# Performance work log

Measured on AMD Instinct MI355X. Metric: run time of the kernel, lower is better.

## Reference

```python
import jax, jax.numpy as jnp
import numpy as np

B, S, F, H = 64, 100, 128, 8
D = F // H
SCALE = D ** -0.5


def setup_inputs() -> dict:
    key = jax.random.key(0)
    ks = jax.random.split(key, 12)
    def lin(k, fan_in, fan_out):
        bound = 1.0 / np.sqrt(fan_in)
        kw, kb = jax.random.split(k)
        W = jax.random.uniform(kw, (fan_in, fan_out), minval=-bound, maxval=bound, dtype=jnp.float32)
        b = jax.random.uniform(kb, (fan_out,), minval=-bound, maxval=bound, dtype=jnp.float32)
        return W, b
    Wq, bq = lin(ks[0], F, F)
    Wk, bk = lin(ks[1], F, F)
    Wv, bv = lin(ks[2], F, F)
    Wo, bo = lin(ks[3], F, F)
    q = jax.random.normal(ks[4], (B, S, F), dtype=jnp.float32)
    k = jax.random.normal(ks[5], (B, S, F), dtype=jnp.float32)
    v = jax.random.normal(ks[6], (B, S, F), dtype=jnp.float32)
    # causal mask broadcast over heads: 1 = keep, 0 = masked
    mask = jnp.tril(jnp.ones((S, S), dtype=jnp.float32))[None, None, :, :].repeat(B, axis=0)
    return {"q": q, "k": k, "v": v, "mask": mask,
            "Wq": Wq, "bq": bq, "Wk": Wk, "bk": bk,
            "Wv": Wv, "bv": bv, "Wo": Wo, "bo": bo}


def reference(q, k, v, mask, Wq, bq, Wk, bk, Wv, bv, Wo, bo):
    # project and split heads: [B,S,F] -> [B,H,S,D]
    def heads(x, W, b):
        y = x @ W + b
        return y.reshape(B, S, H, D).transpose(0, 2, 1, 3)
    qh = heads(q, Wq, bq)
    kh = heads(k, Wk, bk)
    vh = heads(v, Wv, bv)
    scores = jnp.einsum('bhqd,bhkd->bhqk', qh, kh) * SCALE
    scores = jnp.where(mask == 0, -1e9, scores)
    attn = jax.nn.softmax(scores, axis=-1)
    out = jnp.einsum('bhqk,bhkd->bhqd', attn, vh)
    out = out.transpose(0, 2, 1, 3).reshape(B, S, F)
    return out @ Wo + bo
```

## Files before the change

### kernel.cpp

```cpp
#include <hip/hip_runtime.h>
#include <hip/hip_bf16.h>

typedef __attribute__((ext_vector_type(8))) short bf16x8;
typedef __attribute__((ext_vector_type(4))) float f32x4;
typedef __attribute__((ext_vector_type(4))) unsigned short us4;

#define Bb 64
#define Ss 100
#define Ff 128
#define Hh 8
#define Dd 16
#define ROWS (Bb * Ss)
#define ELEMS (ROWS * Ff)

__device__ __forceinline__ unsigned short f2bf(float f) {
    unsigned u = __float_as_uint(f);
    u += 0x7FFFu + ((u >> 16) & 1u);
    return (unsigned short)(u >> 16);
}

__global__ __launch_bounds__(256) void convert_w_kernel(
    const float* __restrict__ Wq, const float* __restrict__ Wk,
    const float* __restrict__ Wv, const float* __restrict__ Wo,
    unsigned short* __restrict__ Wt)
{
    const int wsel = blockIdx.x >> 3, kb = blockIdx.x & 7;
    const float* W = wsel == 0 ? Wq : wsel == 1 ? Wk : wsel == 2 ? Wv : Wo;
    unsigned short* T = Wt + wsel * 16384;
    const int t = threadIdx.x;
    const int n  = t >> 1;
    const int k0 = kb * 16 + (t & 1) * 8;
    bf16x8 v;
#pragma unroll
    for (int j = 0; j < 8; ++j) v[j] = (short)f2bf(W[(k0 + j) * Ff + n]);
    *(bf16x8*)&T[n * Ff + k0] = v;
}

__device__ __forceinline__ void mfma_gemm(const unsigned short* Xs,
                                          const unsigned short* Ws,
                                          f32x4 acc[8], int w, int m, int g)
{
#pragma unroll
    for (int kk = 0; kk < 128; kk += 32) {
        bf16x8 a = *(const bf16x8*)&Xs[(w * 16 + m) * 136 + kk + g * 8];
#pragma unroll
        for (int n = 0; n < 8; ++n) {
            bf16x8 b = *(const bf16x8*)&Ws[(n * 16 + m) * 136 + kk + g * 8];
            acc[n] = __builtin_amdgcn_mfma_f32_16x16x32_bf16(a, b, acc[n], 0, 0, 0);
        }
    }
}

__global__ __launch_bounds__(256) void proj_qkv_kernel(
    const float* __restrict__ q, const float* __restrict__ k, const float* __restrict__ v,
    const unsigned short* __restrict__ Wt,
    const float* __restrict__ bq, const float* __restrict__ bk, const float* __restrict__ bv,
    unsigned short* __restrict__ Qh, unsigned short* __restrict__ Kh, unsigned short* __restrict__ Vh)
{
    __shared__ unsigned short Xs[64 * 136];
    __shared__ unsigned short Ws[128 * 136];
    const int p = blockIdx.y;
    const float* X               = p == 0 ? q  : p == 1 ? k  : v;
    const unsigned short* Wg     = Wt + p * 16384;
    const float* bias            = p == 0 ? bq : p == 1 ? bk : bv;
    unsigned short* OUT          = p == 0 ? Qh : p == 1 ? Kh : Vh;
    const int t = threadIdx.x;
    const int r0 = blockIdx.x * 64;

#pragma unroll
    for (int i = 0; i < 8; ++i) {
        int idx = t + i * 256;
        int r = idx >> 5, c4 = (idx & 31) * 4;
        float4 xv = *(const float4*)&X[(r0 + r) * Ff + c4];
        us4 s4;
        s4[0] = f2bf(xv.x); s4[1] = f2bf(xv.y);
        s4[2] = f2bf(xv.z); s4[3] = f2bf(xv.w);
        *(us4*)&Xs[r * 136 + c4] = s4;
    }
#pragma unroll
    for (int i = 0; i < 8; ++i) {
        int r = (t >> 4) + i * 16, c8 = (t & 15) * 8;
        *(bf16x8*)&Ws[r * 136 + c8] = *(const bf16x8*)&Wg[r * Ff + c8];
    }
    __syncthreads();

    const int w = t >> 6, lane = t & 63, m = lane & 15, g = lane >> 4;
    f32x4 zz = {0.f, 0.f, 0.f, 0.f};
    f32x4 acc[8];
#pragma unroll
    for (int n = 0; n < 8; ++n) acc[n] = zz;
    mfma_gemm(Xs, Ws, acc, w, m, g);

#pragma unroll
    for (int n = 0; n < 8; ++n) {
        float bb = bias[n * 16 + m];
#pragma unroll
        for (int r = 0; r < 4; ++r) {
            int row = r0 + w * 16 + g * 4 + r;
            unsigned b = (unsigned)row / 100u;
            unsigned s = (unsigned)row - b * 100u;
            OUT[((b * 8u + n) * 100u + s) * 16u + m] = f2bf(acc[n][r] + bb);
        }
    }
}

__global__ __launch_bounds__(448) void attn_kernel(
    const unsigned short* __restrict__ Qh, const unsigned short* __restrict__ Kh,
    const unsigned short* __restrict__ Vh, unsigned short* __restrict__ ao)
{
    __shared__ unsigned short lds[24576];
    unsigned short* Qs = lds;
    unsigned short* Ks = lds + 3584;
    unsigned short* Vt = lds + 7168;
    unsigned short* Ps = lds + 9344;

    const int bh = blockIdx.x, b = bh >> 3, h = bh & 7;
    const int t = threadIdx.x;

    for (int i = t; i < 3072; i += 448) ((int4*)lds)[i] = make_int4(0, 0, 0, 0);
    __syncthreads();

    const unsigned short* Qg = Qh + bh * 1600;
    const unsigned short* Kg = Kh + bh * 1600;
    const unsigned short* Vg = Vh + bh * 1600;
    for (int i = t; i < 400; i += 448) {
        int s = i >> 2, d0 = (i & 3) * 4;
        *(us4*)&Qs[s * 32 + d0] = *(const us4*)&Qg[i * 4];
        *(us4*)&Ks[s * 32 + d0] = *(const us4*)&Kg[i * 4];
        us4 vv = *(const us4*)&Vg[i * 4];
        Vt[(d0 + 0) * 136 + s] = vv[0];
        Vt[(d0 + 1) * 136 + s] = vv[1];
        Vt[(d0 + 2) * 136 + s] = vv[2];
        Vt[(d0 + 3) * 136 + s] = vv[3];
    }
    __syncthreads();

    const int w = t >> 6, lane = t & 63, m = lane & 15, g = lane >> 4;
    f32x4 zz = {0.f, 0.f, 0.f, 0.f};

    bf16x8 aq = *(const bf16x8*)&Qs[(w * 16 + m) * 32 + g * 8];
    f32x4 sc[7];
#pragma unroll
    for (int tt = 0; tt < 7; ++tt) {
        bf16x8 bk = *(const bf16x8*)&Ks[(tt * 16 + m) * 32 + g * 8];
        sc[tt] = __builtin_amdgcn_mfma_f32_16x16x32_bf16(aq, bk, zz, 0, 0, 0);
    }

    const int rbase = w * 16 + g * 4;
    float mx[4], sum[4], invl[4];
#pragma unroll
    for (int r = 0; r < 4; ++r) mx[r] = -3.0e38f;
#pragma unroll
    for (int tt = 0; tt < 7; ++tt)
#pragma unroll
        for (int r = 0; r < 4; ++r) {
            float sv = (tt * 16 + m <= rbase + r) ? sc[tt][r] * 0.25f : -1.0e30f;
            sc[tt][r] = sv;
            mx[r] = fmaxf(mx[r], sv);
        }
#pragma unroll
    for (int off = 1; off < 16; off <<= 1)
#pragma unroll
        for (int r = 0; r < 4; ++r) mx[r] = fmaxf(mx[r], __shfl_xor(mx[r], off));
#pragma unroll
    for (int r = 0; r < 4; ++r) sum[r] = 0.f;

    unsigned short* Pw = Ps + w * 2176;
#pragma unroll
    for (int tt = 0; tt < 7; ++tt)
#pragma unroll
        for (int r = 0; r < 4; ++r) {
            float e = __expf(sc[tt][r] - mx[r]);
            sum[r] += e;
            Pw[(g * 4 + r) * 136 + tt * 16 + m] = f2bf(e);
        }
#pragma unroll
    for (int off = 1; off < 16; off <<= 1)
#pragma unroll
        for (int r = 0; r < 4; ++r) sum[r] += __shfl_xor(sum[r], off);
#pragma unroll
    for (int r = 0; r < 4; ++r) invl[r] = 1.0f / sum[r];

    f32x4 oacc = zz;
#pragma unroll
    for (int kk = 0; kk < 128; kk += 32) {
        bf16x8 ap = *(const bf16x8*)&Pw[m * 136 + kk + g * 8];
        bf16x8 bv = *(const bf16x8*)&Vt[m * 136 + kk + g * 8];
        oacc = __builtin_amdgcn_mfma_f32_16x16x32_bf16(ap, bv, oacc, 0, 0, 0);
    }
#pragma unroll
    for (int r = 0; r < 4; ++r) {
        int s = rbase + r;
        if (s < Ss)
            ao[(b * Ss + s) * Ff + h * 16 + m] = f2bf(oacc[r] * invl[r]);
    }
}

__global__ __launch_bounds__(256) void proj_out_kernel(
    const unsigned short* __restrict__ ao, const unsigned short* __restrict__ WtO,
    const float* __restrict__ bo, float* __restrict__ out)
{
    __shared__ unsigned short Xs[64 * 136];
    __shared__ unsigned short Ws[128 * 136];
    const int t = threadIdx.x;
    const int r0 = blockIdx.x * 64;
#pragma unroll
    for (int i = 0; i < 4; ++i) {
        int idx = t + i * 256;
        int r = idx >> 4, c8 = (idx & 15) * 8;
        *(bf16x8*)&Xs[r * 136 + c8] = *(const bf16x8*)&ao[(r0 + r) * Ff + c8];
    }
#pragma unroll
    for (int i = 0; i < 8; ++i) {
        int r = (t >> 4) + i * 16, c8 = (t & 15) * 8;
        *(bf16x8*)&Ws[r * 136 + c8] = *(const bf16x8*)&WtO[r * Ff + c8];
    }
    __syncthreads();

    const int w = t >> 6, lane = t & 63, m = lane & 15, g = lane >> 4;
    f32x4 zz = {0.f, 0.f, 0.f, 0.f};
    f32x4 acc[8];
#pragma unroll
    for (int n = 0; n < 8; ++n) acc[n] = zz;
    mfma_gemm(Xs, Ws, acc, w, m, g);

#pragma unroll
    for (int n = 0; n < 8; ++n) {
        float bb = bo[n * 16 + m];
#pragma unroll
        for (int r = 0; r < 4; ++r) {
            int row = r0 + w * 16 + g * 4 + r;
            out[row * Ff + n * 16 + m] = acc[n][r] + bb;
        }
    }
}

extern "C" void kernel_launch(void* const* d_in, const int* in_sizes, int n_in,
                              void* d_out, int out_size, void* d_ws, size_t ws_size,
                              hipStream_t stream) {
    const float* q  = (const float*)d_in[0];
    const float* k  = (const float*)d_in[1];
    const float* v  = (const float*)d_in[2];
    const float* Wq = (const float*)d_in[4];
    const float* bq = (const float*)d_in[5];
    const float* Wk = (const float*)d_in[6];
    const float* bk = (const float*)d_in[7];
    const float* Wv = (const float*)d_in[8];
    const float* bv = (const float*)d_in[9];
    const float* Wo = (const float*)d_in[10];
    const float* bo = (const float*)d_in[11];

    float* out = (float*)d_out;
    unsigned short* wsu = (unsigned short*)d_ws;
    unsigned short* Wt = wsu;
    unsigned short* Qh = wsu + 65536;
    unsigned short* Kh = Qh + ELEMS;
    unsigned short* Vh = Kh + ELEMS;
    unsigned short* ao = Vh + ELEMS;

    convert_w_kernel<<<dim3(32), dim3(256), 0, stream>>>(Wq, Wk, Wv, Wo, Wt);
    proj_qkv_kernel<<<dim3(100, 3), dim3(256), 0, stream>>>(
        q, k, v, Wt, bq, bk, bv, Qh, Kh, Vh);
    attn_kernel<<<dim3(512), dim3(448), 0, stream>>>(Qh, Kh, Vh, ao);
    proj_out_kernel<<<dim3(100), dim3(256), 0, stream>>>(ao, Wt + 3 * 16384, bo, out);
}
```

Before: 98.29 us.

## Fuse QKV projection into per-head attention kernel and fold weight conversion

Merges the QKV projection into the attention kernel. Each (batch, head) block now loads its 16-column slices of Wq/Wk/Wv, projects q/k/v rows straight from fp32 global memory with MFMA, and keeps Q, K and transposed V in LDS. The Wo transpose and conversion moves into 8 extra blocks of the same launch. This removes two launches and the Qh/Kh/Vh round trip through global memory. In exchange, each head block re-reads the full q/k/v rows, so global input traffic rises about 8x across heads, and it does strided scalar weight loads and a larger LDS footprint.

```diff
diff --git a/kernel.cpp b/kernel.cpp
--- a/kernel.cpp
+++ b/kernel.cpp
@@ -3,13 +3,11 @@
 
 typedef __attribute__((ext_vector_type(8))) short bf16x8;
 typedef __attribute__((ext_vector_type(4))) float f32x4;
-typedef __attribute__((ext_vector_type(4))) unsigned short us4;
 
 #define Bb 64
 #define Ss 100
 #define Ff 128
 #define Hh 8
-#define Dd 16
 #define ROWS (Bb * Ss)
 #define ELEMS (ROWS * Ff)
 
@@ -19,131 +17,97 @@
     return (unsigned short)(u >> 16);
 }
 
-__global__ __launch_bounds__(256) void convert_w_kernel(
-    const float* __restrict__ Wq, const float* __restrict__ Wk,
-    const float* __restrict__ Wv, const float* __restrict__ Wo,
-    unsigned short* __restrict__ Wt)
+__device__ __forceinline__ bf16x8 load_a8(const float* p) {
+    float4 x0 = *(const float4*)p;
+    float4 x1 = *(const float4*)(p + 4);
+    bf16x8 a;
+    a[0] = (short)f2bf(x0.x); a[1] = (short)f2bf(x0.y);
+    a[2] = (short)f2bf(x0.z); a[3] = (short)f2bf(x0.w);
+    a[4] = (short)f2bf(x1.x); a[5] = (short)f2bf(x1.y);
+    a[6] = (short)f2bf(x1.z); a[7] = (short)f2bf(x1.w);
+    return a;
+}
+
+__global__ __launch_bounds__(448) void fused_qkv_attn_kernel(
+    const float* __restrict__ q, const float* __restrict__ k, const float* __restrict__ v,
+    const float* __restrict__ Wq, const float* __restrict__ bq,
+    const float* __restrict__ Wk, const float* __restrict__ bk,
+    const float* __restrict__ Wv, const float* __restrict__ bv,
+    const float* __restrict__ Wo,
+    unsigned short* __restrict__ ao, unsigned short* __restrict__ WtO)
 {
-    const int wsel = blockIdx.x >> 3, kb = blockIdx.x & 7;
-    const float* W = wsel == 0 ? Wq : wsel == 1 ? Wk : wsel == 2 ? Wv : Wo;
-    unsigned short* T = Wt + wsel * 16384;
+    const int blk = blockIdx.x;
     const int t = threadIdx.x;
-    const int n  = t >> 1;
-    const int k0 = kb * 16 + (t & 1) * 8;
-    bf16x8 v;
-#pragma unroll
-    for (int j = 0; j < 8; ++j) v[j] = (short)f2bf(W[(k0 + j) * Ff + n]);
-    *(bf16x8*)&T[n * Ff + k0] = v;
-}
-
-__device__ __forceinline__ void mfma_gemm(const unsigned short* Xs,
-                                          const unsigned short* Ws,
-                                          f32x4 acc[8], int w, int m, int g)
-{
-#pragma unroll
-    for (int kk = 0; kk < 128; kk += 32) {
-        bf16x8 a = *(const bf16x8*)&Xs[(w * 16 + m) * 136 + kk + g * 8];
-#pragma unroll
-        for (int n = 0; n < 8; ++n) {
-            bf16x8 b = *(const bf16x8*)&Ws[(n * 16 + m) * 136 + kk + g * 8];
-            acc[n] = __builtin_amdgcn_mfma_f32_16x16x32_bf16(a, b, acc[n], 0, 0, 0);
-        }
-    }
-}
-
-__global__ __launch_bounds__(256) void proj_qkv_kernel(
-    const float* __restrict__ q, const float* __restrict__ k, const float* __restrict__ v,
-    const unsigned short* __restrict__ Wt,
-    const float* __restrict__ bq, const float* __restrict__ bk, const float* __restrict__ bv,
-    unsigned short* __restrict__ Qh, unsigned short* __restrict__ Kh, unsigned short* __restrict__ Vh)
-{
-    __shared__ unsigned short Xs[64 * 136];
-    __shared__ unsigned short Ws[128 * 136];
-    const int p = blockIdx.y;
-    const float* X               = p == 0 ? q  : p == 1 ? k  : v;
-    const unsigned short* Wg     = Wt + p * 16384;
-    const float* bias            = p == 0 ? bq : p == 1 ? bk : bv;
-    unsigned short* OUT          = p == 0 ? Qh : p == 1 ? Kh : Vh;
-    const int t = threadIdx.x;
-    const int r0 = blockIdx.x * 64;
-
-#pragma unroll
-    for (int i = 0; i < 8; ++i) {
-        int idx = t + i * 256;
-        int r = idx >> 5, c4 = (idx & 31) * 4;
-        float4 xv = *(const float4*)&X[(r0 + r) * Ff + c4];
-        us4 s4;
-        s4[0] = f2bf(xv.x); s4[1] = f2bf(xv.y);
-        s4[2] = f2bf(xv.z); s4[3] = f2bf(xv.w);
-        *(us4*)&Xs[r * 136 + c4] = s4;
-    }
-#pragma unroll
-    for (int i = 0; i < 8; ++i) {
-        int r = (t >> 4) + i * 16, c8 = (t & 15) * 8;
-        *(bf16x8*)&Ws[r * 136 + c8] = *(const bf16x8*)&Wg[r * Ff + c8];
+
+    if (blk >= Bb * Hh) {
+        if (t < 256) {
+            const int kb = blk - Bb * Hh;
+            const int n  = t >> 1;
+            const int k0 = kb * 16 + (t & 1) * 8;
+            bf16x8 vv;
+#pragma unroll
+            for (int j = 0; j < 8; ++j) vv[j] = (short)f2bf(Wo[(k0 + j) * Ff + n]);
+            *(bf16x8*)&WtO[n * Ff + k0] = vv;
+        }
+        return;
+    }
+
+    __shared__ unsigned short lds[32896];
+    const int b = blk >> 3, h = blk & 7;
+
+    {
+        int4* z = (int4*)&lds[6528];
+        for (int i = t; i < 3296; i += 448) z[i] = make_int4(0, 0, 0, 0);
+    }
+    for (int i = t; i < 3 * 2048; i += 448) {
+        const int p = i >> 11, rem = i & 2047;
+        const int kk = rem >> 4, n = rem & 15;
+        const float* Wp = p == 0 ? Wq : p == 1 ? Wk : Wv;
+        lds[p * 2176 + n * 136 + kk] = f2bf(Wp[kk * Ff + h * 16 + n]);
     }
     __syncthreads();
 
     const int w = t >> 6, lane = t & 63, m = lane & 15, g = lane >> 4;
     f32x4 zz = {0.f, 0.f, 0.f, 0.f};
-    f32x4 acc[8];
-#pragma unroll
-    for (int n = 0; n < 8; ++n) acc[n] = zz;
-    mfma_gemm(Xs, Ws, acc, w, m, g);
-
-#pragma unroll
-    for (int n = 0; n < 8; ++n) {
-        float bb = bias[n * 16 + m];
-#pragma unroll
-        for (int r = 0; r < 4; ++r) {
-            int row = r0 + w * 16 + g * 4 + r;
-            unsigned b = (unsigned)row / 100u;
-            unsigned s = (unsigned)row - b * 100u;
-            OUT[((b * 8u + n) * 100u + s) * 16u + m] = f2bf(acc[n][r] + bb);
-        }
-    }
-}
-
-__global__ __launch_bounds__(448) void attn_kernel(
-    const unsigned short* __restrict__ Qh, const unsigned short* __restrict__ Kh,
-    const unsigned short* __restrict__ Vh, unsigned short* __restrict__ ao)
-{
-    __shared__ unsigned short lds[24576];
-    unsigned short* Qs = lds;
-    unsigned short* Ks = lds + 3584;
-    unsigned short* Vt = lds + 7168;
-    unsigned short* Ps = lds + 9344;
-
-    const int bh = blockIdx.x, b = bh >> 3, h = bh & 7;
-    const int t = threadIdx.x;
-
-    for (int i = t; i < 3072; i += 448) ((int4*)lds)[i] = make_int4(0, 0, 0, 0);
+
+    const int rowb = w * 16 + m;
+    const int rowc = rowb < Ss ? rowb : Ss - 1;
+    const float* xq = q + (b * Ss + rowc) * Ff + g * 8;
+    const float* xk = k + (b * Ss + rowc) * Ff + g * 8;
+    const float* xv = v + (b * Ss + rowc) * Ff + g * 8;
+
+    f32x4 accq = zz, acck = zz, accv = zz;
+#pragma unroll
+    for (int kk = 0; kk < 4; ++kk) {
+        const int xo = kk * 32;
+        const int wo = m * 136 + kk * 32 + g * 8;
+        bf16x8 bqf = *(const bf16x8*)&lds[wo];
+        bf16x8 bkf = *(const bf16x8*)&lds[2176 + wo];
+        bf16x8 bvf = *(const bf16x8*)&lds[4352 + wo];
+        accq = __builtin_amdgcn_mfma_f32_16x16x32_bf16(load_a8(xq + xo), bqf, accq, 0, 0, 0);
+        acck = __builtin_amdgcn_mfma_f32_16x16x32_bf16(load_a8(xk + xo), bkf, acck, 0, 0, 0);
+        accv = __builtin_amdgcn_mfma_f32_16x16x32_bf16(load_a8(xv + xo), bvf, accv, 0, 0, 0);
+    }
+    {
+        const float bbq = bq[h * 16 + m];
+        const float bbk = bk[h * 16 + m];
+        const float bbv = bv[h * 16 + m];
+#pragma unroll
+        for (int r = 0; r < 4; ++r) {
+            const int row = w * 16 + g * 4 + r;
+            lds[6528  + row * 40 + m]  = f2bf(accq[r] + bbq);
+            lds[11008 + row * 40 + m]  = f2bf(acck[r] + bbk);
+            lds[15488 + m * 136 + row] = f2bf(accv[r] + bbv);
+        }
+    }
     __syncthreads();
 
-    const unsigned short* Qg = Qh + bh * 1600;
-    const unsigned short* Kg = Kh + bh * 1600;
-    const unsigned short* Vg = Vh + bh * 1600;
-    for (int i = t; i < 400; i += 448) {
-        int s = i >> 2, d0 = (i & 3) * 4;
-        *(us4*)&Qs[s * 32 + d0] = *(const us4*)&Qg[i * 4];
-        *(us4*)&Ks[s * 32 + d0] = *(const us4*)&Kg[i * 4];
-        us4 vv = *(const us4*)&Vg[i * 4];
-        Vt[(d0 + 0) * 136 + s] = vv[0];
-        Vt[(d0 + 1) * 136 + s] = vv[1];
-        Vt[(d0 + 2) * 136 + s] = vv[2];
-        Vt[(d0 + 3) * 136 + s] = vv[3];
-    }
-    __syncthreads();
-
-    const int w = t >> 6, lane = t & 63, m = lane & 15, g = lane >> 4;
-    f32x4 zz = {0.f, 0.f, 0.f, 0.f};
-
-    bf16x8 aq = *(const bf16x8*)&Qs[(w * 16 + m) * 32 + g * 8];
+    bf16x8 aq = *(const bf16x8*)&lds[6528 + (w * 16 + m) * 40 + g * 8];
     f32x4 sc[7];
 #pragma unroll
     for (int tt = 0; tt < 7; ++tt) {
-        bf16x8 bk = *(const bf16x8*)&Ks[(tt * 16 + m) * 32 + g * 8];
-        sc[tt] = __builtin_amdgcn_mfma_f32_16x16x32_bf16(aq, bk, zz, 0, 0, 0);
+        bf16x8 bkf = *(const bf16x8*)&lds[11008 + (tt * 16 + m) * 40 + g * 8];
+        sc[tt] = __builtin_amdgcn_mfma_f32_16x16x32_bf16(aq, bkf, zz, 0, 0, 0);
     }
 
     const int rbase = w * 16 + g * 4;
@@ -165,7 +129,7 @@
 #pragma unroll
     for (int r = 0; r < 4; ++r) sum[r] = 0.f;
 
-    unsigned short* Pw = Ps + w * 2176;
+    unsigned short* Pw = &lds[17664 + w * 2176];
 #pragma unroll
     for (int tt = 0; tt < 7; ++tt)
 #pragma unroll
@@ -185,12 +149,12 @@
 #pragma unroll
     for (int kk = 0; kk < 128; kk += 32) {
         bf16x8 ap = *(const bf16x8*)&Pw[m * 136 + kk + g * 8];
-        bf16x8 bv = *(const bf16x8*)&Vt[m * 136 + kk + g * 8];
-        oacc = __builtin_amdgcn_mfma_f32_16x16x32_bf16(ap, bv, oacc, 0, 0, 0);
+        bf16x8 bvf = *(const bf16x8*)&lds[15488 + m * 136 + kk + g * 8];
+        oacc = __builtin_amdgcn_mfma_f32_16x16x32_bf16(ap, bvf, oacc, 0, 0, 0);
     }
 #pragma unroll
     for (int r = 0; r < 4; ++r) {
-        int s = rbase + r;
+        const int s = rbase + r;
         if (s < Ss)
             ao[(b * Ss + s) * Ff + h * 16 + m] = f2bf(oacc[r] * invl[r]);
     }
@@ -222,7 +186,15 @@
     f32x4 acc[8];
 #pragma unroll
     for (int n = 0; n < 8; ++n) acc[n] = zz;
-    mfma_gemm(Xs, Ws, acc, w, m, g);
+#pragma unroll
+    for (int kk = 0; kk < 128; kk += 32) {
+        bf16x8 a = *(const bf16x8*)&Xs[(w * 16 + m) * 136 + kk + g * 8];
+#pragma unroll
+        for (int n = 0; n < 8; ++n) {
+            bf16x8 bf = *(const bf16x8*)&Ws[(n * 16 + m) * 136 + kk + g * 8];
+            acc[n] = __builtin_amdgcn_mfma_f32_16x16x32_bf16(a, bf, acc[n], 0, 0, 0);
+        }
+    }
 
 #pragma unroll
     for (int n = 0; n < 8; ++n) {
@@ -252,15 +224,10 @@
 
     float* out = (float*)d_out;
     unsigned short* wsu = (unsigned short*)d_ws;
-    unsigned short* Wt = wsu;
-    unsigned short* Qh = wsu + 65536;
-    unsigned short* Kh = Qh + ELEMS;
-    unsigned short* Vh = Kh + ELEMS;
-    unsigned short* ao = Vh + ELEMS;
-
-    convert_w_kernel<<<dim3(32), dim3(256), 0, stream>>>(Wq, Wk, Wv, Wo, Wt);
-    proj_qkv_kernel<<<dim3(100, 3), dim3(256), 0, stream>>>(
-        q, k, v, Wt, bq, bk, bv, Qh, Kh, Vh);
-    attn_kernel<<<dim3(512), dim3(448), 0, stream>>>(Qh, Kh, Vh, ao);
-    proj_out_kernel<<<dim3(100), dim3(256), 0, stream>>>(ao, Wt + 3 * 16384, bo, out);
-}
+    unsigned short* WtO = wsu;
+    unsigned short* ao  = wsu + 16384;
+
+    fused_qkv_attn_kernel<<<dim3(Bb * Hh + 8), dim3(448), 0, stream>>>(
+        q, k, v, Wq, bq, Wk, bk, Wv, bv, Wo, ao, WtO);
+    proj_out_kernel<<<dim3(100), dim3(256), 0, stream>>>(ao, WtO, bo, out);
+}
```

Result: slower. 101.7 us (+3.4%).
